# Optimization experiments

Hardware: AMD Instinct MI355X
Metric: run time of the kernel (lower is better)

## Reference

```python
import jax, jax.numpy as jnp
import numpy as np

PAD_LABEL = 15
NUM_TAGS = 15


def setup_inputs() -> dict:
    key = jax.random.key(0)
    k1, k2, k3 = jax.random.split(key, 3)
    B, T, C = 4096, 512, NUM_TAGS
    logits = jax.random.normal(k1, (B, T, C), dtype=jnp.float32)
    y_true = jax.random.randint(k2, (B, T), 0, PAD_LABEL + 1, dtype=jnp.int32)
    # CRF transition matrix (learned param), glorot-ish scale
    transitions = jax.random.normal(k3, (C, C), dtype=jnp.float32) * 0.25
    return {"logits": logits, "y_true": y_true, "transitions": transitions}


def _log_norm(logits, transitions, mask):
    # logits: (B, T, C) float32, mask: (B, T) bool
    alpha0 = logits[:, 0, :]                       # (B, C)
    # scan over timesteps 1..T-1
    emits = jnp.swapaxes(logits[:, 1:, :], 0, 1)    # (T-1, B, C)
    masks = jnp.swapaxes(mask[:, 1:], 0, 1)         # (T-1, B)

    def step(alpha, inp):
        emit_t, mask_t = inp                        # (B, C), (B,)
        # scores[b, i, j] = alpha[b, i] + trans[i, j] + emit_t[b, j]
        scores = alpha[:, :, None] + transitions[None, :, :] + emit_t[:, None, :]
        new_alpha = jax.scipy.special.logsumexp(scores, axis=1)  # (B, C)
        alpha = jnp.where(mask_t[:, None], new_alpha, alpha)
        return alpha, None

    alpha, _ = jax.lax.scan(step, alpha0, (emits, masks))
    return jax.scipy.special.logsumexp(alpha, axis=1)  # (B,)


def _sequence_score(logits, transitions, labels, mask):
    mask_f = mask.astype(jnp.float32)
    safe_labels = jnp.where(mask, labels, 0)                    # (B, T)
    # emission scores along gold path
    em = jnp.take_along_axis(logits, safe_labels[:, :, None], axis=2)[:, :, 0]
    emission_score = jnp.sum(em * mask_f, axis=1)               # (B,)
    # transition scores between consecutive valid positions
    prev, curr = safe_labels[:, :-1], safe_labels[:, 1:]
    tmask_f = (mask[:, 1:] & mask[:, :-1]).astype(jnp.float32)
    trans_scores = transitions[prev, curr]                      # (B, T-1)
    transition_score = jnp.sum(trans_scores * tmask_f, axis=1)  # (B,)
    return emission_score + transition_score


def reference(logits, y_true, transitions):
    mask = y_true != PAD_LABEL                                  # (B, T) bool
    logZ = _log_norm(logits, transitions, mask)
    path_score = _sequence_score(logits, transitions, y_true, mask)
    nll = jnp.clip(logZ - path_score, 0.0, 1000000.0)
    return jnp.mean(nll)
```

## Files before the change

### kernel.cpp

```cpp
#include <hip/hip_runtime.h>

#define L2E  1.4426950408889634f
#define LN2f 0.6931471805599453f

template<int CTRL>
__device__ __forceinline__ float dppf(float x) {
  int r = __builtin_amdgcn_update_dpp(0, __builtin_bit_cast(int, x), CTRL, 0xF, 0xF, true);
  return __builtin_bit_cast(float, r);
}
template<int CTRL>
__device__ __forceinline__ int dppi(int x) {
  return __builtin_amdgcn_update_dpp(0, x, CTRL, 0xF, 0xF, true);
}

__device__ __forceinline__ float bflymax16(float x) {
  x = fmaxf(x, dppf<0xB1>(x));
  x = fmaxf(x, dppf<0x4E>(x));
  x = fmaxf(x, dppf<0x141>(x));
  x = fmaxf(x, dppf<0x140>(x));
  return x;
}

#define DOT(shv, tot) {                                   \
    float t0_ = (shv) * Wror[0], t1_ = 0.f, t2_ = 0.f, t3_ = 0.f; \
    t1_ = fmaf(dppf<0x121>(shv), Wror[1],  t1_);          \
    t2_ = fmaf(dppf<0x122>(shv), Wror[2],  t2_);          \
    t3_ = fmaf(dppf<0x123>(shv), Wror[3],  t3_);          \
    t0_ = fmaf(dppf<0x124>(shv), Wror[4],  t0_);          \
    t1_ = fmaf(dppf<0x125>(shv), Wror[5],  t1_);          \
    t2_ = fmaf(dppf<0x126>(shv), Wror[6],  t2_);          \
    t3_ = fmaf(dppf<0x127>(shv), Wror[7],  t3_);          \
    t0_ = fmaf(dppf<0x128>(shv), Wror[8],  t0_);          \
    t1_ = fmaf(dppf<0x129>(shv), Wror[9],  t1_);          \
    t2_ = fmaf(dppf<0x12A>(shv), Wror[10], t2_);          \
    t3_ = fmaf(dppf<0x12B>(shv), Wror[11], t3_);          \
    t0_ = fmaf(dppf<0x12C>(shv), Wror[12], t0_);          \
    t1_ = fmaf(dppf<0x12D>(shv), Wror[13], t1_);          \
    t2_ = fmaf(dppf<0x12E>(shv), Wror[14], t2_);          \
    t3_ = fmaf(dppf<0x12F>(shv), Wror[15], t3_);          \
    tot = (t0_ + t1_) + (t2_ + t3_); }

#define VWAIT(N) do { asm volatile("s_waitcnt vmcnt(" #N ")" ::: "memory"); \
                      __builtin_amdgcn_sched_barrier(0); } while (0)
#define SBAR()   __builtin_amdgcn_sched_barrier(0)

#define FSTEP(emit, yi, RN) do {                                      \
    const float e_ = (emit); const int yi_ = (yi);                    \
    const float p_ = exp2f(e_ * L2E);                                 \
    float tot_; DOT(own, tot_);                                       \
    const float cand_ = tot_ * p_;                                    \
    own = (yi_ != 15) ? cand_ : own;                                  \
    eacc += (yi_ == jm) ? e_ : 0.f;                                   \
    if (RN) { const float m_ = bflymax16(own);                        \
      own *= __builtin_amdgcn_rcpf(m_); M += log2f(m_); }             \
  } while (0)

#define BSTEP(emit, yi, RN) do {                                      \
    const float e_ = (emit); const int yi_ = (yi);                    \
    const float p_ = exp2f(e_ * L2E);                                 \
    const float sh_ = own * p_;                                       \
    float tot_; DOT(sh_, tot_);                                       \
    own = (yi_ != 15) ? tot_ : own;                                   \
    eacc += (yi_ == jm) ? e_ : 0.f;                                   \
    if (RN) { const float m_ = bflymax16(own);                        \
      own *= __builtin_amdgcn_rcpf(m_); M += log2f(m_); }             \
  } while (0)

#define FISS(EB, Y0, Y1) do {                                         \
    EB[0] = *(const float*)(eub + evoff);                             \
    EB[1] = *(const float*)(eub + evoff + 60);                        \
    EB[2] = *(const float*)(eub + evoff + 120);                       \
    EB[3] = *(const float*)(eub + evoff + 180);                       \
    EB[4] = *(const float*)(eub + evoff + 240);                       \
    EB[5] = *(const float*)(eub + evoff + 300);                       \
    EB[6] = *(const float*)(eub + evoff + 360);                       \
    EB[7] = *(const float*)(eub + evoff + 420);                       \
    Y0 = *(const int4*)(yub + yvoff);                                 \
    Y1 = *(const int4*)(yub + yvoff + 16);                            \
    evoff += 480; yvoff += 32;                                        \
  } while (0)

#define BISS(EB, Y0, Y1) do {                                         \
    EB[0] = *(const float*)(eub + evoff);                             \
    EB[1] = *(const float*)(eub + evoff - 60);                        \
    EB[2] = *(const float*)(eub + evoff - 120);                       \
    EB[3] = *(const float*)(eub + evoff - 180);                       \
    EB[4] = *(const float*)(eub + evoff - 240);                       \
    EB[5] = *(const float*)(eub + evoff - 300);                       \
    EB[6] = *(const float*)(eub + evoff - 360);                       \
    EB[7] = *(const float*)(eub + evoff - 420);                       \
    Y0 = *(const int4*)(yub + yvoff);                                 \
    Y1 = *(const int4*)(yub + yvoff + 16);                            \
    evoff -= 480; yvoff -= 32;                                        \
  } while (0)

#define FCONS(EB, Y0, Y1) do {                                        \
    FSTEP(EB[0], (Y0).x, 0); FSTEP(EB[1], (Y0).y, 0);                 \
    FSTEP(EB[2], (Y0).z, 0); FSTEP(EB[3], (Y0).w, 0);                 \
    FSTEP(EB[4], (Y1).x, 0); FSTEP(EB[5], (Y1).y, 0);                 \
    FSTEP(EB[6], (Y1).z, 0); FSTEP(EB[7], (Y1).w, 1);                 \
  } while (0)

#define BCONS(EB, Y0, Y1) do {                                        \
    BSTEP(EB[0], (Y1).w, 0); BSTEP(EB[1], (Y1).z, 0);                 \
    BSTEP(EB[2], (Y1).y, 0); BSTEP(EB[3], (Y1).x, 0);                 \
    BSTEP(EB[4], (Y0).w, 0); BSTEP(EB[5], (Y0).z, 0);                 \
    BSTEP(EB[6], (Y0).y, 0); BSTEP(EB[7], (Y0).x, 1);                 \
  } while (0)

__global__ __launch_bounds__(256, 2)
void crf_batch(const float* __restrict__ logits, const int* __restrict__ yg,
               const float* __restrict__ trans, float* __restrict__ out) {
  __shared__ float Tl[240];
  __shared__ float comb[8][2][16];
  __shared__ float pathE[8][2];
  __shared__ float transS[8];
  __shared__ float blks[8];

  const int tid = threadIdx.x;
  if (tid < 225) Tl[tid] = trans[tid];
  __syncthreads();

  const char* eub = (const char*)logits + (size_t)blockIdx.x * (8 * 30720);
  const char* yub = (const char*)yg + (size_t)blockIdx.x * (8 * 2048);

  {
    const int q = tid >> 5, l32 = tid & 31;
    const int* ys = (const int*)(yub + q * 2048);
    float acc = 0.f;
    #pragma unroll
    for (int m = 0; m < 16; ++m) {
      const int t = 1 + l32 + 32 * m;
      if (t < 512) {
        const int yc = ys[t], yp = ys[t - 1];
        if (yc < 15 && yp < 15) acc += Tl[yp * 15 + yc];
      }
    }
    #pragma unroll
    for (int k = 1; k < 32; k <<= 1) acc += __shfl_xor(acc, k, 32);
    if (l32 == 0) transS[q] = acc;
  }

  const int wave = tid >> 6, lane = tid & 63;
  const int j = lane & 15;
  const int sLoc = (wave >> 1) * 4 + (lane >> 4);
  const bool isFwd = (wave & 1) == 0;
  const int jj = (j < 15) ? j : 14;
  const int jm = (j < 15) ? j : 255;
  const int sBase = sLoc * 30720;
  const int yBase = sLoc * 2048;

  float Wror[16];
  Wror[0] = (j < 15) ? exp2f(Tl[j * 16] * L2E) : 0.f;
#define SETW(R) { const int s_ = dppi<0x120 + (R)>(j);                  \
    const bool v_ = (j < 15) && (s_ < 15);                              \
    const int ix_ = isFwd ? s_ * 15 + j : j * 15 + s_;                  \
    Wror[R] = v_ ? exp2f(Tl[v_ ? ix_ : 0] * L2E) : 0.f; }
  SETW(1)  SETW(2)  SETW(3)  SETW(4)  SETW(5)
  SETW(6)  SETW(7)  SETW(8)  SETW(9)  SETW(10)
  SETW(11) SETW(12) SETW(13) SETW(14) SETW(15)
#undef SETW
  #pragma unroll
  for (int r = 0; r < 16; ++r) asm volatile("" : "+v"(Wror[r]));

  float own, M, eacc;
  float ebA[8], ebB[8];
  int4 yA0, yA1, yB0, yB1;

  if (isFwd) {
    int evoff = sBase + jj * 4;
    int yvoff = yBase;
    float e0[8];
    #pragma unroll
    for (int i = 0; i < 8; ++i) e0[i] = *(const float*)(eub + evoff + i * 60);
    const int4 yP0 = *(const int4*)(yub + yvoff);
    const int4 yP1 = *(const int4*)(yub + yvoff + 16);
    evoff += 480; yvoff += 32;
    FISS(ebA, yA0, yA1);
    FISS(ebB, yB0, yB1);
    SBAR();

    const float a0 = e0[0];
    eacc = (yP0.x == jm) ? a0 : 0.f;
    const float A = (j < 15) ? a0 * L2E : -1.0e30f;
    const float M0 = bflymax16(A);
    own = exp2f(A - M0);
    M = M0;
    FSTEP(e0[1], yP0.y, 0); FSTEP(e0[2], yP0.z, 0); FSTEP(e0[3], yP0.w, 0);
    FSTEP(e0[4], yP1.x, 0); FSTEP(e0[5], yP1.y, 0); FSTEP(e0[6], yP1.z, 0);
    FSTEP(e0[7], yP1.w, 1);

    #pragma unroll 1
    for (int k = 0; k < 14; ++k) {
      VWAIT(10); FCONS(ebA, yA0, yA1); FISS(ebA, yA0, yA1); SBAR();
      VWAIT(10); FCONS(ebB, yB0, yB1); FISS(ebB, yB0, yB1); SBAR();
    }
    VWAIT(10); FCONS(ebA, yA0, yA1); FISS(ebA, yA0, yA1); SBAR();
    VWAIT(10); FCONS(ebB, yB0, yB1);
    VWAIT(0);  FCONS(ebA, yA0, yA1);
  } else {
    int evoff = sBase + jj * 4 + 511 * 60;
    int yvoff = yBase + 504 * 4;
    own = (j < 15) ? 1.f : 0.f;
    M = 0.f; eacc = 0.f;
    BISS(ebA, yA0, yA1);
    BISS(ebB, yB0, yB1);
    SBAR();
    #pragma unroll 1
    for (int k = 0; k < 15; ++k) {
      VWAIT(10); BCONS(ebA, yA0, yA1); BISS(ebA, yA0, yA1); SBAR();
      VWAIT(10); BCONS(ebB, yB0, yB1); BISS(ebB, yB0, yB1); SBAR();
    }
    VWAIT(10); BCONS(ebA, yA0, yA1);
    VWAIT(0);  BCONS(ebB, yB0, yB1);
  }

  const int dir = isFwd ? 0 : 1;
  if (j < 15) comb[sLoc][dir][j] = M + log2f(own);
  #pragma unroll
  for (int k = 1; k < 16; k <<= 1) eacc += __shfl_xor(eacc, k, 16);
  if (j == 0) pathE[sLoc][dir] = eacc;

  __syncthreads();

  if (tid < 8) {
    float mx = -3.0e38f; float s[15];
    #pragma unroll
    for (int i = 0; i < 15; ++i) {
      s[i] = comb[tid][0][i] + comb[tid][1][i];
      mx = fmaxf(mx, s[i]);
    }
    float sum = 0.f;
    #pragma unroll
    for (int i = 0; i < 15; ++i) sum += exp2f(s[i] - mx);
    const float logZ = (mx + log2f(sum)) * LN2f;
    const float path = pathE[tid][0] + pathE[tid][1] + transS[tid];
    float nll = logZ - path;
    nll = fminf(fmaxf(nll, 0.f), 1000000.f);
    blks[tid] = nll;
  }
  __syncthreads();
  if (tid == 0) {
    const float tot = (blks[0] + blks[1]) + (blks[2] + blks[3]) +
                      (blks[4] + blks[5]) + (blks[6] + blks[7]);
    atomicAdd(out, tot * (1.0f / 4096.0f));
  }
}

extern "C" void kernel_launch(void* const* d_in, const int* in_sizes, int n_in,
                              void* d_out, int out_size, void* d_ws, size_t ws_size,
                              hipStream_t stream) {
  const float* logits = (const float*)d_in[0];
  const int*   y      = (const int*)d_in[1];
  const float* trans  = (const float*)d_in[2];
  float* out = (float*)d_out;

  hipMemsetAsync(out, 0, sizeof(float), stream);

  const int B = in_sizes[1] / 512;
  crf_batch<<<dim3(B / 8), dim3(256), 0, stream>>>(logits, y, trans, out);
}
```

Baseline: 61.34 us.

## Interleave two independent sequences per lane group for instruction-level parallelism

```diff
diff --git a/kernel.cpp b/kernel.cpp
--- a/kernel.cpp
+++ b/kernel.cpp
@@ -44,111 +44,120 @@
                       __builtin_amdgcn_sched_barrier(0); } while (0)
 #define SBAR()   __builtin_amdgcn_sched_barrier(0)
 
-#define FSTEP(emit, yi, RN) do {                                      \
+#define FSTEP(OWN, MM, EAC, emit, yi, RN) do {                        \
     const float e_ = (emit); const int yi_ = (yi);                    \
     const float p_ = exp2f(e_ * L2E);                                 \
-    float tot_; DOT(own, tot_);                                       \
+    float tot_; DOT(OWN, tot_);                                       \
     const float cand_ = tot_ * p_;                                    \
-    own = (yi_ != 15) ? cand_ : own;                                  \
-    eacc += (yi_ == jm) ? e_ : 0.f;                                   \
-    if (RN) { const float m_ = bflymax16(own);                        \
-      own *= __builtin_amdgcn_rcpf(m_); M += log2f(m_); }             \
-  } while (0)
-
-#define BSTEP(emit, yi, RN) do {                                      \
+    OWN = (yi_ != 15) ? cand_ : OWN;                                  \
+    EAC += (yi_ == jm) ? e_ : 0.f;                                    \
+    if (RN) { const float m_ = bflymax16(OWN);                        \
+      OWN *= __builtin_amdgcn_rcpf(m_); MM += log2f(m_); }            \
+  } while (0)
+
+#define BSTEP(OWN, MM, EAC, emit, yi, RN) do {                        \
     const float e_ = (emit); const int yi_ = (yi);                    \
     const float p_ = exp2f(e_ * L2E);                                 \
-    const float sh_ = own * p_;                                       \
+    const float sh_ = OWN * p_;                                       \
     float tot_; DOT(sh_, tot_);                                       \
-    own = (yi_ != 15) ? tot_ : own;                                   \
-    eacc += (yi_ == jm) ? e_ : 0.f;                                   \
-    if (RN) { const float m_ = bflymax16(own);                        \
-      own *= __builtin_amdgcn_rcpf(m_); M += log2f(m_); }             \
-  } while (0)
-
-#define FISS(EB, Y0, Y1) do {                                         \
-    EB[0] = *(const float*)(eub + evoff);                             \
-    EB[1] = *(const float*)(eub + evoff + 60);                        \
-    EB[2] = *(const float*)(eub + evoff + 120);                       \
-    EB[3] = *(const float*)(eub + evoff + 180);                       \
-    EB[4] = *(const float*)(eub + evoff + 240);                       \
-    EB[5] = *(const float*)(eub + evoff + 300);                       \
-    EB[6] = *(const float*)(eub + evoff + 360);                       \
-    EB[7] = *(const float*)(eub + evoff + 420);                       \
-    Y0 = *(const int4*)(yub + yvoff);                                 \
-    Y1 = *(const int4*)(yub + yvoff + 16);                            \
-    evoff += 480; yvoff += 32;                                        \
-  } while (0)
-
-#define BISS(EB, Y0, Y1) do {                                         \
-    EB[0] = *(const float*)(eub + evoff);                             \
-    EB[1] = *(const float*)(eub + evoff - 60);                        \
-    EB[2] = *(const float*)(eub + evoff - 120);                       \
-    EB[3] = *(const float*)(eub + evoff - 180);                       \
-    EB[4] = *(const float*)(eub + evoff - 240);                       \
-    EB[5] = *(const float*)(eub + evoff - 300);                       \
-    EB[6] = *(const float*)(eub + evoff - 360);                       \
-    EB[7] = *(const float*)(eub + evoff - 420);                       \
-    Y0 = *(const int4*)(yub + yvoff);                                 \
-    Y1 = *(const int4*)(yub + yvoff + 16);                            \
-    evoff -= 480; yvoff -= 32;                                        \
-  } while (0)
-
-#define FCONS(EB, Y0, Y1) do {                                        \
-    FSTEP(EB[0], (Y0).x, 0); FSTEP(EB[1], (Y0).y, 0);                 \
-    FSTEP(EB[2], (Y0).z, 0); FSTEP(EB[3], (Y0).w, 0);                 \
-    FSTEP(EB[4], (Y1).x, 0); FSTEP(EB[5], (Y1).y, 0);                 \
-    FSTEP(EB[6], (Y1).z, 0); FSTEP(EB[7], (Y1).w, 1);                 \
-  } while (0)
-
-#define BCONS(EB, Y0, Y1) do {                                        \
-    BSTEP(EB[0], (Y1).w, 0); BSTEP(EB[1], (Y1).z, 0);                 \
-    BSTEP(EB[2], (Y1).y, 0); BSTEP(EB[3], (Y1).x, 0);                 \
-    BSTEP(EB[4], (Y0).w, 0); BSTEP(EB[5], (Y0).z, 0);                 \
-    BSTEP(EB[6], (Y0).y, 0); BSTEP(EB[7], (Y0).x, 1);                 \
-  } while (0)
-
-__global__ __launch_bounds__(256, 2)
-void crf_batch(const float* __restrict__ logits, const int* __restrict__ yg,
-               const float* __restrict__ trans, float* __restrict__ out) {
+    OWN = (yi_ != 15) ? tot_ : OWN;                                   \
+    EAC += (yi_ == jm) ? e_ : 0.f;                                    \
+    if (RN) { const float m_ = bflymax16(OWN);                        \
+      OWN *= __builtin_amdgcn_rcpf(m_); MM += log2f(m_); }            \
+  } while (0)
+
+#define FISSV(EBF, Y0, Y1, EV, YV) do {                               \
+    EBF[0] = *(const float*)(eub + EV);                               \
+    EBF[1] = *(const float*)(eub + EV + 60);                          \
+    EBF[2] = *(const float*)(eub + EV + 120);                         \
+    EBF[3] = *(const float*)(eub + EV + 180);                         \
+    EBF[4] = *(const float*)(eub + EV + 240);                         \
+    EBF[5] = *(const float*)(eub + EV + 300);                         \
+    EBF[6] = *(const float*)(eub + EV + 360);                         \
+    EBF[7] = *(const float*)(eub + EV + 420);                         \
+    Y0 = *(const int4*)(yub + YV);                                    \
+    Y1 = *(const int4*)(yub + YV + 16);                               \
+    EV += 480; YV += 32;                                              \
+  } while (0)
+
+#define BISSV(EBF, Y0, Y1, EV, YV) do {                               \
+    EBF[0] = *(const float*)(eub + EV);                               \
+    EBF[1] = *(const float*)(eub + EV - 60);                          \
+    EBF[2] = *(const float*)(eub + EV - 120);                         \
+    EBF[3] = *(const float*)(eub + EV - 180);                         \
+    EBF[4] = *(const float*)(eub + EV - 240);                         \
+    EBF[5] = *(const float*)(eub + EV - 300);                         \
+    EBF[6] = *(const float*)(eub + EV - 360);                         \
+    EBF[7] = *(const float*)(eub + EV - 420);                         \
+    Y0 = *(const int4*)(yub + YV);                                    \
+    Y1 = *(const int4*)(yub + YV + 16);                               \
+    EV -= 480; YV -= 32;                                              \
+  } while (0)
+
+#define PFCONS(EA, YA0, YA1, EBB, YB0, YB1) do {                                  \
+    FSTEP(ownA,MA,eaccA, EA[0], (YA0).x, 0); FSTEP(ownB,MB,eaccB, EBB[0], (YB0).x, 0); \
+    FSTEP(ownA,MA,eaccA, EA[1], (YA0).y, 0); FSTEP(ownB,MB,eaccB, EBB[1], (YB0).y, 0); \
+    FSTEP(ownA,MA,eaccA, EA[2], (YA0).z, 0); FSTEP(ownB,MB,eaccB, EBB[2], (YB0).z, 0); \
+    FSTEP(ownA,MA,eaccA, EA[3], (YA0).w, 0); FSTEP(ownB,MB,eaccB, EBB[3], (YB0).w, 0); \
+    FSTEP(ownA,MA,eaccA, EA[4], (YA1).x, 0); FSTEP(ownB,MB,eaccB, EBB[4], (YB1).x, 0); \
+    FSTEP(ownA,MA,eaccA, EA[5], (YA1).y, 0); FSTEP(ownB,MB,eaccB, EBB[5], (YB1).y, 0); \
+    FSTEP(ownA,MA,eaccA, EA[6], (YA1).z, 0); FSTEP(ownB,MB,eaccB, EBB[6], (YB1).z, 0); \
+    FSTEP(ownA,MA,eaccA, EA[7], (YA1).w, 1); FSTEP(ownB,MB,eaccB, EBB[7], (YB1).w, 1); \
+  } while (0)
+
+#define PBCONS(EA, YA0, YA1, EBB, YB0, YB1) do {                                  \
+    BSTEP(ownA,MA,eaccA, EA[0], (YA1).w, 0); BSTEP(ownB,MB,eaccB, EBB[0], (YB1).w, 0); \
+    BSTEP(ownA,MA,eaccA, EA[1], (YA1).z, 0); BSTEP(ownB,MB,eaccB, EBB[1], (YB1).z, 0); \
+    BSTEP(ownA,MA,eaccA, EA[2], (YA1).y, 0); BSTEP(ownB,MB,eaccB, EBB[2], (YB1).y, 0); \
+    BSTEP(ownA,MA,eaccA, EA[3], (YA1).x, 0); BSTEP(ownB,MB,eaccB, EBB[3], (YB1).x, 0); \
+    BSTEP(ownA,MA,eaccA, EA[4], (YA0).w, 0); BSTEP(ownB,MB,eaccB, EBB[4], (YB0).w, 0); \
+    BSTEP(ownA,MA,eaccA, EA[5], (YA0).z, 0); BSTEP(ownB,MB,eaccB, EBB[5], (YB0).z, 0); \
+    BSTEP(ownA,MA,eaccA, EA[6], (YA0).y, 0); BSTEP(ownB,MB,eaccB, EBB[6], (YB0).y, 0); \
+    BSTEP(ownA,MA,eaccA, EA[7], (YA0).x, 1); BSTEP(ownB,MB,eaccB, EBB[7], (YB0).x, 1); \
+  } while (0)
+
+__global__ __launch_bounds__(256, 1)
+void crf_ilp(const float* __restrict__ logits, const int* __restrict__ yg,
+             const float* __restrict__ trans, float* __restrict__ out) {
   __shared__ float Tl[240];
-  __shared__ float comb[8][2][16];
-  __shared__ float pathE[8][2];
-  __shared__ float transS[8];
-  __shared__ float blks[8];
+  __shared__ float comb[16][2][16];
+  __shared__ float pathE[16][2];
+  __shared__ float transS[16];
+  __shared__ float blks[16];
 
   const int tid = threadIdx.x;
   if (tid < 225) Tl[tid] = trans[tid];
   __syncthreads();
 
-  const char* eub = (const char*)logits + (size_t)blockIdx.x * (8 * 30720);
-  const char* yub = (const char*)yg + (size_t)blockIdx.x * (8 * 2048);
+  const char* eub = (const char*)logits + (size_t)blockIdx.x * (16 * 30720);
+  const char* yub = (const char*)yg + (size_t)blockIdx.x * (16 * 2048);
 
   {
-    const int q = tid >> 5, l32 = tid & 31;
-    const int* ys = (const int*)(yub + q * 2048);
+    const int sq = tid >> 4, l16 = tid & 15;
+    const int* ys = (const int*)(yub + sq * 2048);
     float acc = 0.f;
     #pragma unroll
-    for (int m = 0; m < 16; ++m) {
-      const int t = 1 + l32 + 32 * m;
+    for (int m = 0; m < 32; ++m) {
+      const int t = 1 + l16 + 16 * m;
       if (t < 512) {
         const int yc = ys[t], yp = ys[t - 1];
         if (yc < 15 && yp < 15) acc += Tl[yp * 15 + yc];
       }
     }
     #pragma unroll
-    for (int k = 1; k < 32; k <<= 1) acc += __shfl_xor(acc, k, 32);
-    if (l32 == 0) transS[q] = acc;
+    for (int k = 1; k < 16; k <<= 1) acc += __shfl_xor(acc, k, 16);
+    if (l16 == 0) transS[sq] = acc;
   }
 
   const int wave = tid >> 6, lane = tid & 63;
   const int j = lane & 15;
-  const int sLoc = (wave >> 1) * 4 + (lane >> 4);
-  const bool isFwd = (wave & 1) == 0;
+  const int c = lane >> 4;
+  const bool isFwd = (wave >> 1) == 0;
+  const int half = wave & 1;
+  const int sA = half * 8 + c;
+  const int sB = half * 8 + 4 + c;
   const int jj = (j < 15) ? j : 14;
   const int jm = (j < 15) ? j : 255;
-  const int sBase = sLoc * 30720;
-  const int yBase = sLoc * 2048;
 
   float Wror[16];
   Wror[0] = (j < 15) ? exp2f(Tl[j * 16] * L2E) : 0.f;
@@ -163,67 +172,93 @@
   #pragma unroll
   for (int r = 0; r < 16; ++r) asm volatile("" : "+v"(Wror[r]));
 
-  float own, M, eacc;
-  float ebA[8], ebB[8];
-  int4 yA0, yA1, yB0, yB1;
+  float ownA, MA, eaccA, ownB, MB, eaccB;
+  float ebXA[8], ebYA[8], ebXB[8], ebYB[8];
+  int4 yXA0, yXA1, yYA0, yYA1, yXB0, yXB1, yYB0, yYB1;
 
   if (isFwd) {
-    int evoff = sBase + jj * 4;
-    int yvoff = yBase;
-    float e0[8];
-    #pragma unroll
-    for (int i = 0; i < 8; ++i) e0[i] = *(const float*)(eub + evoff + i * 60);
-    const int4 yP0 = *(const int4*)(yub + yvoff);
-    const int4 yP1 = *(const int4*)(yub + yvoff + 16);
-    evoff += 480; yvoff += 32;
-    FISS(ebA, yA0, yA1);
-    FISS(ebB, yB0, yB1);
+    int evA = sA * 30720 + jj * 4, yvA = sA * 2048;
+    int evB = sB * 30720 + jj * 4, yvB = sB * 2048;
+    float e0A[8], e0B[8];
+    #pragma unroll
+    for (int i = 0; i < 8; ++i) {
+      e0A[i] = *(const float*)(eub + evA + i * 60);
+      e0B[i] = *(const float*)(eub + evB + i * 60);
+    }
+    const int4 yPA0 = *(const int4*)(yub + yvA);
+    const int4 yPA1 = *(const int4*)(yub + yvA + 16);
+    const int4 yPB0 = *(const int4*)(yub + yvB);
+    const int4 yPB1 = *(const int4*)(yub + yvB + 16);
+    evA += 480; yvA += 32; evB += 480; yvB += 32;
+    FISSV(ebXA, yXA0, yXA1, evA, yvA);
+    FISSV(ebXB, yXB0, yXB1, evB, yvB);
+    FISSV(ebYA, yYA0, yYA1, evA, yvA);
+    FISSV(ebYB, yYB0, yYB1, evB, yvB);
     SBAR();
 
-    const float a0 = e0[0];
-    eacc = (yP0.x == jm) ? a0 : 0.f;
-    const float A = (j < 15) ? a0 * L2E : -1.0e30f;
-    const float M0 = bflymax16(A);
-    own = exp2f(A - M0);
-    M = M0;
-    FSTEP(e0[1], yP0.y, 0); FSTEP(e0[2], yP0.z, 0); FSTEP(e0[3], yP0.w, 0);
-    FSTEP(e0[4], yP1.x, 0); FSTEP(e0[5], yP1.y, 0); FSTEP(e0[6], yP1.z, 0);
-    FSTEP(e0[7], yP1.w, 1);
+    const float a0A = e0A[0], a0B = e0B[0];
+    eaccA = (yPA0.x == jm) ? a0A : 0.f;
+    eaccB = (yPB0.x == jm) ? a0B : 0.f;
+    const float AA = (j < 15) ? a0A * L2E : -1.0e30f;
+    const float AB = (j < 15) ? a0B * L2E : -1.0e30f;
+    const float M0A = bflymax16(AA), M0B = bflymax16(AB);
+    ownA = exp2f(AA - M0A); MA = M0A;
+    ownB = exp2f(AB - M0B); MB = M0B;
+    FSTEP(ownA,MA,eaccA, e0A[1], yPA0.y, 0); FSTEP(ownB,MB,eaccB, e0B[1], yPB0.y, 0);
+    FSTEP(ownA,MA,eaccA, e0A[2], yPA0.z, 0); FSTEP(ownB,MB,eaccB, e0B[2], yPB0.z, 0);
+    FSTEP(ownA,MA,eaccA, e0A[3], yPA0.w, 0); FSTEP(ownB,MB,eaccB, e0B[3], yPB0.w, 0);
+    FSTEP(ownA,MA,eaccA, e0A[4], yPA1.x, 0); FSTEP(ownB,MB,eaccB, e0B[4], yPB1.x, 0);
+    FSTEP(ownA,MA,eaccA, e0A[5], yPA1.y, 0); FSTEP(ownB,MB,eaccB, e0B[5], yPB1.y, 0);
+    FSTEP(ownA,MA,eaccA, e0A[6], yPA1.z, 0); FSTEP(ownB,MB,eaccB, e0B[6], yPB1.z, 0);
+    FSTEP(ownA,MA,eaccA, e0A[7], yPA1.w, 1); FSTEP(ownB,MB,eaccB, e0B[7], yPB1.w, 1);
 
     #pragma unroll 1
     for (int k = 0; k < 14; ++k) {
-      VWAIT(10); FCONS(ebA, yA0, yA1); FISS(ebA, yA0, yA1); SBAR();
-      VWAIT(10); FCONS(ebB, yB0, yB1); FISS(ebB, yB0, yB1); SBAR();
-    }
-    VWAIT(10); FCONS(ebA, yA0, yA1); FISS(ebA, yA0, yA1); SBAR();
-    VWAIT(10); FCONS(ebB, yB0, yB1);
-    VWAIT(0);  FCONS(ebA, yA0, yA1);
+      VWAIT(20); PFCONS(ebXA,yXA0,yXA1, ebXB,yXB0,yXB1);
+      FISSV(ebXA,yXA0,yXA1,evA,yvA); FISSV(ebXB,yXB0,yXB1,evB,yvB); SBAR();
+      VWAIT(20); PFCONS(ebYA,yYA0,yYA1, ebYB,yYB0,yYB1);
+      FISSV(ebYA,yYA0,yYA1,evA,yvA); FISSV(ebYB,yYB0,yYB1,evB,yvB); SBAR();
+    }
+    VWAIT(20); PFCONS(ebXA,yXA0,yXA1, ebXB,yXB0,yXB1);
+    FISSV(ebXA,yXA0,yXA1,evA,yvA); FISSV(ebXB,yXB0,yXB1,evB,yvB); SBAR();
+    VWAIT(20); PFCONS(ebYA,yYA0,yYA1, ebYB,yYB0,yYB1);
+    VWAIT(0);  PFCONS(ebXA,yXA0,yXA1, ebXB,yXB0,yXB1);
   } else {
-    int evoff = sBase + jj * 4 + 511 * 60;
-    int yvoff = yBase + 504 * 4;
-    own = (j < 15) ? 1.f : 0.f;
-    M = 0.f; eacc = 0.f;
-    BISS(ebA, yA0, yA1);
-    BISS(ebB, yB0, yB1);
+    int evA = sA * 30720 + jj * 4 + 511 * 60, yvA = sA * 2048 + 504 * 4;
+    int evB = sB * 30720 + jj * 4 + 511 * 60, yvB = sB * 2048 + 504 * 4;
+    ownA = (j < 15) ? 1.f : 0.f; MA = 0.f; eaccA = 0.f;
+    ownB = (j < 15) ? 1.f : 0.f; MB = 0.f; eaccB = 0.f;
+    BISSV(ebXA, yXA0, yXA1, evA, yvA);
+    BISSV(ebXB, yXB0, yXB1, evB, yvB);
+    BISSV(ebYA, yYA0, yYA1, evA, yvA);
+    BISSV(ebYB, yYB0, yYB1, evB, yvB);
     SBAR();
     #pragma unroll 1
     for (int k = 0; k < 15; ++k) {
-      VWAIT(10); BCONS(ebA, yA0, yA1); BISS(ebA, yA0, yA1); SBAR();
-      VWAIT(10); BCONS(ebB, yB0, yB1); BISS(ebB, yB0, yB1); SBAR();
-    }
-    VWAIT(10); BCONS(ebA, yA0, yA1);
-    VWAIT(0);  BCONS(ebB, yB0, yB1);
+      VWAIT(20); PBCONS(ebXA,yXA0,yXA1, ebXB,yXB0,yXB1);
+      BISSV(ebXA,yXA0,yXA1,evA,yvA); BISSV(ebXB,yXB0,yXB1,evB,yvB); SBAR();
+      VWAIT(20); PBCONS(ebYA,yYA0,yYA1, ebYB,yYB0,yYB1);
+      BISSV(ebYA,yYA0,yYA1,evA,yvA); BISSV(ebYB,yYB0,yYB1,evB,yvB); SBAR();
+    }
+    VWAIT(20); PBCONS(ebXA,yXA0,yXA1, ebXB,yXB0,yXB1);
+    VWAIT(0);  PBCONS(ebYA,yYA0,yYA1, ebYB,yYB0,yYB1);
   }
 
   const int dir = isFwd ? 0 : 1;
-  if (j < 15) comb[sLoc][dir][j] = M + log2f(own);
+  if (j < 15) {
+    comb[sA][dir][j] = MA + log2f(ownA);
+    comb[sB][dir][j] = MB + log2f(ownB);
+  }
   #pragma unroll
-  for (int k = 1; k < 16; k <<= 1) eacc += __shfl_xor(eacc, k, 16);
-  if (j == 0) pathE[sLoc][dir] = eacc;
+  for (int k = 1; k < 16; k <<= 1) {
+    eaccA += __shfl_xor(eaccA, k, 16);
+    eaccB += __shfl_xor(eaccB, k, 16);
+  }
+  if (j == 0) { pathE[sA][dir] = eaccA; pathE[sB][dir] = eaccB; }
 
   __syncthreads();
 
-  if (tid < 8) {
+  if (tid < 16) {
     float mx = -3.0e38f; float s[15];
     #pragma unroll
     for (int i = 0; i < 15; ++i) {
@@ -241,8 +276,9 @@
   }
   __syncthreads();
   if (tid == 0) {
-    const float tot = (blks[0] + blks[1]) + (blks[2] + blks[3]) +
-                      (blks[4] + blks[5]) + (blks[6] + blks[7]);
+    float tot = 0.f;
+    #pragma unroll
+    for (int i = 0; i < 16; ++i) tot += blks[i];
     atomicAdd(out, tot * (1.0f / 4096.0f));
   }
 }
@@ -258,5 +294,5 @@
   hipMemsetAsync(out, 0, sizeof(float), stream);
 
   const int B = in_sizes[1] / 512;
-  crf_batch<<<dim3(B / 8), dim3(256), 0, stream>>>(logits, y, trans, out);
-}
+  crf_ilp<<<dim3(B / 16), dim3(256), 0, stream>>>(logits, y, trans, out);
+}
```

Result: slower. 67.02 us (+9.3%).
